# Kernel optimization log

Hardware: AMD Instinct MI355X
Metric: run time of the kernel (lower is better)

The kernel has to match this reference:

```python
import jax, jax.numpy as jnp
import numpy as np

BITS = 4
GROUP_SIZE = 128
IN_F = 4096
OUT_F = 11008
MAXQ = (1 << BITS) - 1
PACK = 32 // BITS  # 8 values per int32 word


def setup_inputs() -> dict:
    key = jax.random.key(0)
    k1, k2, k3, k4, k5 = jax.random.split(key, 5)
    x = jax.random.normal(k1, (2, 2048, IN_F), dtype=jnp.float32)
    qweight = jax.random.randint(k2, (IN_F // PACK, OUT_F), 0, 2147483647, dtype=jnp.int32)
    qzeros = jax.random.randint(k3, (IN_F // GROUP_SIZE, OUT_F // PACK), 0, 2147483647, dtype=jnp.int32)
    scales = jax.random.uniform(k4, (IN_F // GROUP_SIZE, OUT_F), dtype=jnp.float32) * 0.01 + 1e-4
    bias = jax.random.normal(k5, (OUT_F,), dtype=jnp.float32)
    return {"x": x, "qweight": qweight, "qzeros": qzeros, "scales": scales, "bias": bias}


def _dequant_weight(qweight, qzeros, scales):
    shifts = jnp.arange(0, 32, BITS, dtype=jnp.int32)
    # unpack packed int4 weights: [K/8, N] -> [K/8, 8, N] -> [K, N]
    w = (qweight[:, None, :] >> shifts[None, :, None]) & MAXQ
    w = w.reshape(-1, qweight.shape[-1]).astype(jnp.float32)  # [K, N]
    # unpack zero points: [G, N/8] -> [G, N/8, 8] -> [G, N]
    z = (qzeros[:, :, None] >> shifts[None, None, :]) & MAXQ
    z = z.reshape(qzeros.shape[0], -1).astype(jnp.float32)  # [G, N]
    gidx = jnp.arange(w.shape[0]) // GROUP_SIZE  # [K]
    # asymmetric group-wise dequant: (q - zero) * scale
    return (w - z[gidx]) * scales[gidx].astype(jnp.float32)  # [K, N]


def reference(x, qweight, qzeros, scales, bias):
    raw_dtype = x.dtype
    W = _dequant_weight(qweight, qzeros, scales)  # [K, N] fp32
    x2 = x.astype(jnp.float32).reshape(-1, x.shape[-1])  # [M, K]
    out = x2 @ W + bias.astype(jnp.float32)  # [M, N]
    return out.astype(raw_dtype).reshape(x.shape[:-1] + (W.shape[-1],))
```

## Files before the change

kernel.cpp:

```cpp
#include <hip/hip_runtime.h>
#include <hip/hip_bf16.h>
#include <stdint.h>

#define K_DIM 4096
#define N_DIM 11008
#define GROUP 128

typedef __attribute__((ext_vector_type(8))) __bf16 bf16x8;
typedef __attribute__((ext_vector_type(4))) float f32x4;
typedef __attribute__((address_space(3))) uint8_t lds_u8;
typedef __attribute__((address_space(3))) void lds_void;
typedef __attribute__((address_space(1))) const void g_void;

static __device__ inline __bf16 f2bf(float f) { return (__bf16)f; }

__global__ __launch_bounds__(256) void cvt_x_kernel(const float* __restrict__ x,
                                                    __bf16* __restrict__ xb, int total8) {
    int t = blockIdx.x * 256 + threadIdx.x;
    if (t >= total8) return;
    f32x4 a0 = *(const f32x4*)(x + (size_t)t * 8);
    f32x4 a1 = *(const f32x4*)(x + (size_t)t * 8 + 4);
    bf16x8 v;
    #pragma unroll
    for (int j = 0; j < 4; ++j) { v[j] = f2bf(a0[j]); v[j + 4] = f2bf(a1[j]); }
    *(bf16x8*)(xb + (size_t)t * 8) = v;
}

__global__ __launch_bounds__(256) void dequant_w_kernel(const int* __restrict__ qw,
                                                        const int* __restrict__ qz,
                                                        const float* __restrict__ sc,
                                                        __bf16* __restrict__ wb) {
    const int n   = blockIdx.x * 256 + threadIdx.x;
    const int kb0 = blockIdx.y * 8;
    const int g   = blockIdx.y >> 1;
    const float s   = sc[(size_t)g * N_DIM + n];
    const float nzs = -(float)((qz[(size_t)g * (N_DIM / 8) + (n >> 3)] >> ((n & 7) * 4)) & 15) * s;
    #pragma unroll
    for (int j = 0; j < 8; ++j) {
        const int w = qw[(size_t)(kb0 + j) * N_DIM + n];
        bf16x8 v;
        #pragma unroll
        for (int b = 0; b < 8; ++b)
            v[b] = f2bf(fmaf((float)((w >> (4 * b)) & 15), s, nzs));
        *(bf16x8*)(wb + (size_t)n * K_DIM + (size_t)(kb0 + j) * 8) = v;
    }
}

#define BM2 256
#define BN2 256
#define BK2 64
#define NT  (K_DIM / BK2)

__global__ __launch_bounds__(512, 2) void gemm256_kernel(
    const __bf16* __restrict__ xb, const __bf16* __restrict__ wb,
    const float* __restrict__ bias, float* __restrict__ out)
{
    __shared__ __align__(16) __bf16 As[2][BM2 * BK2];
    __shared__ __align__(16) __bf16 Bs[2][BN2 * BK2];

    const int tid  = threadIdx.x;
    const int lane = tid & 63;
    const int wid  = tid >> 6;
    const int wm = (wid >> 2) * 128;
    const int wn = (wid & 3) * 64;

    const int bid = blockIdx.x;
    const int wg  = (bid & 7) * 86 + (bid >> 3);
    const int m0 = (wg / 43) * BM2;
    const int n0 = (wg % 43) * BN2;

    const __bf16* pa[4];
    const __bf16* pb[4];
    int chk[4];
    #pragma unroll
    for (int l = 0; l < 4; ++l) {
        const int ch  = l * 512 + tid;
        const int row = ch >> 3;
        const int g   = (ch & 7) ^ (row & 7);
        chk[l] = ch;
        pa[l] = xb + (size_t)(m0 + row) * K_DIM + g * 8;
        pb[l] = wb + (size_t)(n0 + row) * K_DIM + g * 8;
    }
    lds_u8* baseA = (lds_u8*)&As[0][0];
    lds_u8* baseB = (lds_u8*)&Bs[0][0];

    auto STAGE_A = [&](int buf, int half, int kofs) {
        lds_u8* d = baseA + buf * (BM2 * BK2 * 2);
        #pragma unroll
        for (int l = half * 2; l < half * 2 + 2; ++l)
            __builtin_amdgcn_global_load_lds((g_void*)(pa[l] + kofs),
                                             (lds_void*)(d + chk[l] * 16), 16, 0, 0);
    };
    auto STAGE_B = [&](int buf, int half, int kofs) {
        lds_u8* d = baseB + buf * (BN2 * BK2 * 2);
        #pragma unroll
        for (int l = half * 2; l < half * 2 + 2; ++l)
            __builtin_amdgcn_global_load_lds((g_void*)(pb[l] + kofs),
                                             (lds_void*)(d + chk[l] * 16), 16, 0, 0);
    };

    const int fr  = lane & 15;
    const int fc  = lane >> 4;
    const int swz = fr & 7;
    const int col0 = (fc ^ swz) * 8;
    const int col1 = ((4 + fc) ^ swz) * 8;
    const int rowoffA = (wm + fr) * BK2;
    const int rowoffB = (wn + fr) * BK2;

    f32x4 acc[8][4];
    #pragma unroll
    for (int m = 0; m < 8; ++m)
        #pragma unroll
        for (int n = 0; n < 4; ++n) acc[m][n] = (f32x4){0.f, 0.f, 0.f, 0.f};

    STAGE_A(0, 0, 0);   STAGE_B(0, 0, 0);   STAGE_A(0, 1, 0);   STAGE_B(0, 1, 0);
    STAGE_A(1, 0, BK2); STAGE_B(1, 0, BK2); STAGE_A(1, 1, BK2); STAGE_B(1, 1, BK2);
    asm volatile("s_waitcnt vmcnt(8)" ::: "memory");
    __builtin_amdgcn_sched_barrier(0);
    __builtin_amdgcn_s_barrier();
    __builtin_amdgcn_sched_barrier(0);

    for (int u = 0; u < NT; ++u) {
        const int cur = u & 1;
        const __bf16* ra = &As[0][0] + cur * (BM2 * BK2) + rowoffA;
        const __bf16* rb = &Bs[0][0] + cur * (BN2 * BK2) + rowoffB;
        const int  pf  = (u + 2) * BK2;
        const bool pfv = (u + 2) < NT;
        bf16x8 aR[8], a2[8], bR[8];

        #pragma unroll
        for (int n = 0; n < 4; ++n) {
            bR[n * 2 + 0] = *(const bf16x8*)(rb + n * 1024 + col0);
            bR[n * 2 + 1] = *(const bf16x8*)(rb + n * 1024 + col1);
        }
        #pragma unroll
        for (int m = 0; m < 4; ++m) {
            aR[m * 2 + 0] = *(const bf16x8*)(ra + m * 1024 + col0);
            aR[m * 2 + 1] = *(const bf16x8*)(ra + m * 1024 + col1);
        }
        __builtin_amdgcn_s_barrier();
        asm volatile("s_waitcnt lgkmcnt(0)" ::: "memory");
        __builtin_amdgcn_sched_barrier(0);
        __builtin_amdgcn_s_setprio(1);
        #pragma unroll
        for (int m = 0; m < 4; ++m)
            #pragma unroll
            for (int n = 0; n < 2; ++n)
                #pragma unroll
                for (int kk = 0; kk < 2; ++kk)
                    acc[m][n] = __builtin_amdgcn_mfma_f32_16x16x32_bf16(
                        aR[m * 2 + kk], bR[n * 2 + kk], acc[m][n], 0, 0, 0);
        __builtin_amdgcn_s_setprio(0);
        __builtin_amdgcn_s_barrier();

        #pragma unroll
        for (int m = 0; m < 4; ++m) {
            a2[m * 2 + 0] = *(const bf16x8*)(ra + (m + 4) * 1024 + col0);
            a2[m * 2 + 1] = *(const bf16x8*)(ra + (m + 4) * 1024 + col1);
        }
        __builtin_amdgcn_s_barrier();
        asm volatile("s_waitcnt lgkmcnt(0)" ::: "memory");
        __builtin_amdgcn_sched_barrier(0);
        __builtin_amdgcn_s_setprio(1);
        #pragma unroll
        for (int m = 0; m < 4; ++m)
            #pragma unroll
            for (int n = 2; n < 4; ++n)
                #pragma unroll
                for (int kk = 0; kk < 2; ++kk)
                    acc[m][n] = __builtin_amdgcn_mfma_f32_16x16x32_bf16(
                        aR[m * 2 + kk], bR[n * 2 + kk], acc[m][n], 0, 0, 0);
        __builtin_amdgcn_s_setprio(0);
        __builtin_amdgcn_sched_barrier(0);
        __builtin_amdgcn_s_barrier();
        __builtin_amdgcn_sched_barrier(0);

        if (pfv) { STAGE_A(cur, 0, pf); STAGE_B(cur, 0, pf); }
        __builtin_amdgcn_s_barrier();
        __builtin_amdgcn_s_setprio(1);
        #pragma unroll
        for (int m = 0; m < 4; ++m)
            #pragma unroll
            for (int n = 0; n < 2; ++n)
                #pragma unroll
                for (int kk = 0; kk < 2; ++kk)
                    acc[m + 4][n] = __builtin_amdgcn_mfma_f32_16x16x32_bf16(
                        a2[m * 2 + kk], bR[n * 2 + kk], acc[m + 4][n], 0, 0, 0);
        __builtin_amdgcn_s_setprio(0);
        __builtin_amdgcn_s_barrier();

        if (pfv) { STAGE_A(cur, 1, pf); STAGE_B(cur, 1, pf); }
        __builtin_amdgcn_s_barrier();
        __builtin_amdgcn_s_setprio(1);
        #pragma unroll
        for (int m = 0; m < 4; ++m)
            #pragma unroll
            for (int n = 2; n < 4; ++n)
                #pragma unroll
                for (int kk = 0; kk < 2; ++kk)
                    acc[m + 4][n] = __builtin_amdgcn_mfma_f32_16x16x32_bf16(
                        a2[m * 2 + kk], bR[n * 2 + kk], acc[m + 4][n], 0, 0, 0);
        __builtin_amdgcn_s_setprio(0);
        if (pfv) { asm volatile("s_waitcnt vmcnt(8)" ::: "memory"); }
        else     { asm volatile("s_waitcnt vmcnt(0)" ::: "memory"); }
        __builtin_amdgcn_sched_barrier(0);
        __builtin_amdgcn_s_barrier();
        __builtin_amdgcn_sched_barrier(0);
    }

    const int cn  = lane & 15;
    const int cr4 = (lane >> 4) * 4;
    #pragma unroll
    for (int n = 0; n < 4; ++n) {
        const int col = n0 + wn + n * 16 + cn;
        const float bv = bias[col];
        #pragma unroll
        for (int m = 0; m < 8; ++m) {
            const int row = m0 + wm + m * 16 + cr4;
            #pragma unroll
            for (int r = 0; r < 4; ++r)
                out[(size_t)(row + r) * N_DIM + col] = acc[m][n][r] + bv;
        }
    }
}

#define FBM 128
#define FBN 128
#define FBK 32
#define FLDSS 40
__global__ __launch_bounds__(256) void gptq_gemm_fused_kernel(
    const float* __restrict__ x, const int* __restrict__ qw, const int* __restrict__ qz,
    const float* __restrict__ sc, const float* __restrict__ bias, float* __restrict__ out)
{
    __shared__ __align__(16) __bf16 Asm[FBM][FLDSS];
    __shared__ __align__(16) __bf16 Bsm[FBN][FLDSS];
    const int tid = threadIdx.x, lane = tid & 63, wid = tid >> 6;
    const int m0 = blockIdx.y * FBM, n0 = blockIdx.x * FBN;
    const int wm = (wid >> 1) * 64, wn = (wid & 1) * 64;
    f32x4 acc[4][4];
    #pragma unroll
    for (int i = 0; i < 4; ++i)
        #pragma unroll
        for (int j = 0; j < 4; ++j) acc[i][j] = (f32x4){0.f, 0.f, 0.f, 0.f};
    const int a_m = tid >> 2, a_h = tid & 3;
    const int b_n = tid & 127, b_k8 = tid >> 7;
    const int ng = n0 + b_n, zsh = (ng & 7) * 4;
    const int fr = lane & 15, fc = lane >> 4;
    for (int k0 = 0; k0 < K_DIM; k0 += FBK) {
        const int g = k0 >> 7;
        const float* xa = x + (size_t)(m0 + a_m) * K_DIM + k0 + a_h * 8;
        f32x4 a0 = *(const f32x4*)xa;
        f32x4 a1 = *(const f32x4*)(xa + 4);
        const float* xbp = xa + (size_t)64 * K_DIM;
        f32x4 a2 = *(const f32x4*)xbp;
        f32x4 a3 = *(const f32x4*)(xbp + 4);
        const int kb = (k0 >> 3) + b_k8;
        const int w0 = qw[(size_t)kb * N_DIM + ng];
        const int w1 = qw[(size_t)(kb + 2) * N_DIM + ng];
        const float s = sc[(size_t)g * N_DIM + ng];
        const float nzs = -(float)((qz[(size_t)g * (N_DIM / 8) + (ng >> 3)] >> zsh) & 15) * s;
        __syncthreads();
        bf16x8 av0, av1;
        #pragma unroll
        for (int j = 0; j < 4; ++j) {
            av0[j] = f2bf(a0[j]); av0[j + 4] = f2bf(a1[j]);
            av1[j] = f2bf(a2[j]); av1[j + 4] = f2bf(a3[j]);
        }
        *(bf16x8*)&Asm[a_m][a_h * 8] = av0;
        *(bf16x8*)&Asm[a_m + 64][a_h * 8] = av1;
        bf16x8 bv0, bv1;
        #pragma unroll
        for (int j = 0; j < 8; ++j) {
            bv0[j] = f2bf(fmaf((float)((w0 >> (4 * j)) & 15), s, nzs));
            bv1[j] = f2bf(fmaf((float)((w1 >> (4 * j)) & 15), s, nzs));
        }
        *(bf16x8*)&Bsm[b_n][b_k8 * 8] = bv0;
        *(bf16x8*)&Bsm[b_n][(b_k8 + 2) * 8] = bv1;
        __syncthreads();
        bf16x8 af[4], bfr[4];
        #pragma unroll
        for (int i = 0; i < 4; ++i) af[i] = *(const bf16x8*)&Asm[wm + i * 16 + fr][fc * 8];
        #pragma unroll
        for (int j = 0; j < 4; ++j) bfr[j] = *(const bf16x8*)&Bsm[wn + j * 16 + fr][fc * 8];
        #pragma unroll
        for (int i = 0; i < 4; ++i)
            #pragma unroll
            for (int j = 0; j < 4; ++j)
                acc[i][j] = __builtin_amdgcn_mfma_f32_16x16x32_bf16(af[i], bfr[j], acc[i][j], 0, 0, 0);
    }
    const int cn = lane & 15, cr4 = (lane >> 4) * 4;
    #pragma unroll
    for (int j = 0; j < 4; ++j) {
        const int col = n0 + wn + j * 16 + cn;
        const float bv = bias[col];
        #pragma unroll
        for (int i = 0; i < 4; ++i) {
            const int row = m0 + wm + i * 16 + cr4;
            #pragma unroll
            for (int r = 0; r < 4; ++r)
                out[(size_t)(row + r) * N_DIM + col] = acc[i][j][r] + bv;
        }
    }
}

extern "C" void kernel_launch(void* const* d_in, const int* in_sizes, int n_in,
                              void* d_out, int out_size, void* d_ws, size_t ws_size,
                              hipStream_t stream) {
    const float* x    = (const float*)d_in[0];
    const int*   qw   = (const int*)d_in[1];
    const int*   qz   = (const int*)d_in[2];
    const float* sc   = (const float*)d_in[3];
    const float* bias = (const float*)d_in[4];
    float* out = (float*)d_out;
    const int M = in_sizes[0] / K_DIM;

    const size_t xb_bytes = (size_t)M * K_DIM * sizeof(__bf16);
    const size_t wb_bytes = (size_t)N_DIM * K_DIM * sizeof(__bf16);
    if (ws_size >= xb_bytes + wb_bytes && (M % BM2) == 0) {
        __bf16* xb = (__bf16*)d_ws;
        __bf16* wb = (__bf16*)((uint8_t*)d_ws + xb_bytes);
        const int total8 = M * K_DIM / 8;
        cvt_x_kernel<<<dim3(total8 / 256), dim3(256), 0, stream>>>(x, xb, total8);
        dequant_w_kernel<<<dim3(N_DIM / 256, K_DIM / 8 / 8), dim3(256), 0, stream>>>(qw, qz, sc, wb);
        const int nblocks = (N_DIM / BN2) * (M / BM2);
        gemm256_kernel<<<dim3(nblocks), dim3(512), 0, stream>>>(xb, wb, bias, out);
    } else {
        gptq_gemm_fused_kernel<<<dim3(N_DIM / FBN, M / FBM), dim3(256), 0, stream>>>(x, qw, qz, sc, bias, out);
    }
}
```

Before: 443.7 us.

## Restructure GEMM main loop into four A-quarter phases with staggered A/B prefetch

Changes the pipeline so A is prefetched one tile ahead into the other buffer, while B stays two tiles ahead in the current buffer. The A fragments are now loaded from LDS in four smaller chunks, each interleaved with its own MFMA block, instead of two big ones. This lowers register pressure from A fragments and spreads global-to-LDS issue across more phases, so more memory traffic can overlap with compute. The risk is a reduced prefetch distance for A and a tighter vmcnt(4) wait, which could expose load latency or cause LDS races if the barriers are not sufficient.

```diff
diff --git a/kernel.cpp b/kernel.cpp
--- a/kernel.cpp
+++ b/kernel.cpp
@@ -113,20 +113,24 @@
         #pragma unroll
         for (int n = 0; n < 4; ++n) acc[m][n] = (f32x4){0.f, 0.f, 0.f, 0.f};
 
-    STAGE_A(0, 0, 0);   STAGE_B(0, 0, 0);   STAGE_A(0, 1, 0);   STAGE_B(0, 1, 0);
-    STAGE_A(1, 0, BK2); STAGE_B(1, 0, BK2); STAGE_A(1, 1, BK2); STAGE_B(1, 1, BK2);
-    asm volatile("s_waitcnt vmcnt(8)" ::: "memory");
+    STAGE_B(0, 0, 0);   STAGE_B(0, 1, 0);
+    STAGE_A(0, 0, 0);   STAGE_A(0, 1, 0);
+    STAGE_B(1, 0, BK2); STAGE_B(1, 1, BK2);
+    asm volatile("s_waitcnt vmcnt(4)" ::: "memory");
     __builtin_amdgcn_sched_barrier(0);
     __builtin_amdgcn_s_barrier();
     __builtin_amdgcn_sched_barrier(0);
 
     for (int u = 0; u < NT; ++u) {
         const int cur = u & 1;
+        const int nc  = cur ^ 1;
         const __bf16* ra = &As[0][0] + cur * (BM2 * BK2) + rowoffA;
         const __bf16* rb = &Bs[0][0] + cur * (BN2 * BK2) + rowoffB;
-        const int  pf  = (u + 2) * BK2;
-        const bool pfv = (u + 2) < NT;
-        bf16x8 aR[8], a2[8], bR[8];
+        const int  kA  = (u + 1) * BK2;
+        const int  kB  = (u + 2) * BK2;
+        const bool pfA = (u + 1) < NT;
+        const bool pfB = (u + 2) < NT;
+        bf16x8 bR[8], a01[4], a23[4], a45[4], a67[4];
 
         #pragma unroll
         for (int n = 0; n < 4; ++n) {
@@ -134,74 +138,88 @@
             bR[n * 2 + 1] = *(const bf16x8*)(rb + n * 1024 + col1);
         }
         #pragma unroll
-        for (int m = 0; m < 4; ++m) {
-            aR[m * 2 + 0] = *(const bf16x8*)(ra + m * 1024 + col0);
-            aR[m * 2 + 1] = *(const bf16x8*)(ra + m * 1024 + col1);
-        }
+        for (int f = 0; f < 2; ++f) {
+            a01[f * 2 + 0] = *(const bf16x8*)(ra + f * 1024 + col0);
+            a01[f * 2 + 1] = *(const bf16x8*)(ra + f * 1024 + col1);
+        }
+        if (pfA) STAGE_A(nc, 0, kA);
         __builtin_amdgcn_s_barrier();
         asm volatile("s_waitcnt lgkmcnt(0)" ::: "memory");
         __builtin_amdgcn_sched_barrier(0);
         __builtin_amdgcn_s_setprio(1);
         #pragma unroll
-        for (int m = 0; m < 4; ++m)
-            #pragma unroll
-            for (int n = 0; n < 2; ++n)
+        for (int f = 0; f < 2; ++f)
+            #pragma unroll
+            for (int n = 0; n < 4; ++n)
                 #pragma unroll
                 for (int kk = 0; kk < 2; ++kk)
-                    acc[m][n] = __builtin_amdgcn_mfma_f32_16x16x32_bf16(
-                        aR[m * 2 + kk], bR[n * 2 + kk], acc[m][n], 0, 0, 0);
+                    acc[f][n] = __builtin_amdgcn_mfma_f32_16x16x32_bf16(
+                        a01[f * 2 + kk], bR[n * 2 + kk], acc[f][n], 0, 0, 0);
         __builtin_amdgcn_s_setprio(0);
         __builtin_amdgcn_s_barrier();
 
         #pragma unroll
-        for (int m = 0; m < 4; ++m) {
-            a2[m * 2 + 0] = *(const bf16x8*)(ra + (m + 4) * 1024 + col0);
-            a2[m * 2 + 1] = *(const bf16x8*)(ra + (m + 4) * 1024 + col1);
-        }
+        for (int f = 0; f < 2; ++f) {
+            a23[f * 2 + 0] = *(const bf16x8*)(ra + (f + 2) * 1024 + col0);
+            a23[f * 2 + 1] = *(const bf16x8*)(ra + (f + 2) * 1024 + col1);
+        }
+        if (pfA) STAGE_A(nc, 1, kA);
+        if (pfB) STAGE_B(cur, 0, kB);
         __builtin_amdgcn_s_barrier();
         asm volatile("s_waitcnt lgkmcnt(0)" ::: "memory");
         __builtin_amdgcn_sched_barrier(0);
         __builtin_amdgcn_s_setprio(1);
         #pragma unroll
-        for (int m = 0; m < 4; ++m)
-            #pragma unroll
-            for (int n = 2; n < 4; ++n)
+        for (int f = 0; f < 2; ++f)
+            #pragma unroll
+            for (int n = 0; n < 4; ++n)
                 #pragma unroll
                 for (int kk = 0; kk < 2; ++kk)
-                    acc[m][n] = __builtin_amdgcn_mfma_f32_16x16x32_bf16(
-                        aR[m * 2 + kk], bR[n * 2 + kk], acc[m][n], 0, 0, 0);
+                    acc[f + 2][n] = __builtin_amdgcn_mfma_f32_16x16x32_bf16(
+                        a23[f * 2 + kk], bR[n * 2 + kk], acc[f + 2][n], 0, 0, 0);
         __builtin_amdgcn_s_setprio(0);
-        __builtin_amdgcn_sched_barrier(0);
-        __builtin_amdgcn_s_barrier();
-        __builtin_amdgcn_sched_barrier(0);
-
-        if (pfv) { STAGE_A(cur, 0, pf); STAGE_B(cur, 0, pf); }
-        __builtin_amdgcn_s_barrier();
+        __builtin_amdgcn_s_barrier();
+
+        #pragma unroll
+        for (int f = 0; f < 2; ++f) {
+            a45[f * 2 + 0] = *(const bf16x8*)(ra + (f + 4) * 1024 + col0);
+            a45[f * 2 + 1] = *(const bf16x8*)(ra + (f + 4) * 1024 + col1);
+        }
+        if (pfB) STAGE_B(cur, 1, kB);
+        __builtin_amdgcn_s_barrier();
+        asm volatile("s_waitcnt lgkmcnt(0)" ::: "memory");
+        __builtin_amdgcn_sched_barrier(0);
         __builtin_amdgcn_s_setprio(1);
         #pragma unroll
-        for (int m = 0; m < 4; ++m)
-            #pragma unroll
-            for (int n = 0; n < 2; ++n)
+        for (int f = 0; f < 2; ++f)
+            #pragma unroll
+            for (int n = 0; n < 4; ++n)
                 #pragma unroll
                 for (int kk = 0; kk < 2; ++kk)
-                    acc[m + 4][n] = __builtin_amdgcn_mfma_f32_16x16x32_bf16(
-                        a2[m * 2 + kk], bR[n * 2 + kk], acc[m + 4][n], 0, 0, 0);
+                    acc[f + 4][n] = __builtin_amdgcn_mfma_f32_16x16x32_bf16(
+                        a45[f * 2 + kk], bR[n * 2 + kk], acc[f + 4][n], 0, 0, 0);
         __builtin_amdgcn_s_setprio(0);
         __builtin_amdgcn_s_barrier();
 
-        if (pfv) { STAGE_A(cur, 1, pf); STAGE_B(cur, 1, pf); }
-        __builtin_amdgcn_s_barrier();
+        #pragma unroll
+        for (int f = 0; f < 2; ++f) {
+            a67[f * 2 + 0] = *(const bf16x8*)(ra + (f + 6) * 1024 + col0);
+            a67[f * 2 + 1] = *(const bf16x8*)(ra + (f + 6) * 1024 + col1);
+        }
+        __builtin_amdgcn_s_barrier();
+        asm volatile("s_waitcnt lgkmcnt(0)" ::: "memory");
+        __builtin_amdgcn_sched_barrier(0);
         __builtin_amdgcn_s_setprio(1);
         #pragma unroll
-        for (int m = 0; m < 4; ++m)
-            #pragma unroll
-            for (int n = 2; n < 4; ++n)
+        for (int f = 0; f < 2; ++f)
+            #pragma unroll
+            for (int n = 0; n < 4; ++n)
                 #pragma unroll
                 for (int kk = 0; kk < 2; ++kk)
-                    acc[m + 4][n] = __builtin_amdgcn_mfma_f32_16x16x32_bf16(
-                        a2[m * 2 + kk], bR[n * 2 + kk], acc[m + 4][n], 0, 0, 0);
+                    acc[f + 6][n] = __builtin_amdgcn_mfma_f32_16x16x32_bf16(
+                        a67[f * 2 + kk], bR[n * 2 + kk], acc[f + 6][n], 0, 0, 0);
         __builtin_amdgcn_s_setprio(0);
-        if (pfv) { asm volatile("s_waitcnt vmcnt(8)" ::: "memory"); }
+        if (pfB) { asm volatile("s_waitcnt vmcnt(4)" ::: "memory"); }
         else     { asm volatile("s_waitcnt vmcnt(0)" ::: "memory"); }
         __builtin_amdgcn_sched_barrier(0);
         __builtin_amdgcn_s_barrier();
```

Result: slower. 473.9 us (+6.8%).
